# Kernel tuning notes

Measured on AMD Instinct MI355X. Metric: run time of the kernel, lower is better.

Reference implementation:

```python
import jax, jax.numpy as jnp
import numpy as np

N = 8192
H = 512
E = 262144
NUM_LAYERS = 2
LAYER_DECAY = 0.4
INIT_W = 1e-05


def setup_inputs() -> dict:
    key = jax.random.key(0)
    ks = jax.random.split(key, 6)
    x = jax.random.normal(ks[0], (N, H), dtype=jnp.float32)
    rows = jax.random.randint(ks[1], (E,), 0, N, dtype=jnp.int32)
    cols = jax.random.randint(ks[2], (E,), 0, N, dtype=jnp.int32)
    vals = jax.random.uniform(ks[3], (E,), dtype=jnp.float32)
    # near-identity init as in GSS_GNNLayer (torch Linear: y = x @ W.T + b)
    W1 = jax.random.normal(ks[4], (H, H), dtype=jnp.float32) * INIT_W + jnp.eye(H, dtype=jnp.float32)
    b1 = jnp.zeros((H,), dtype=jnp.float32)
    W2 = jax.random.normal(ks[5], (H, H), dtype=jnp.float32) * INIT_W + jnp.eye(H, dtype=jnp.float32)
    b2 = jnp.zeros((H,), dtype=jnp.float32)
    return {"x": x, "rows": rows, "cols": cols, "vals": vals,
            "W1": W1, "b1": b1, "W2": W2, "b2": b2}


def _spmm(rows, cols, vals, dense):
    # sparse [N,N] @ dense [N,H] via gather + segment-sum scatter-add
    return jax.ops.segment_sum(vals[:, None] * dense[cols], rows, num_segments=N)


def _gcn_layer(x, rows, cols, vals, W1, b1, W2, b2):
    Ax = _spmm(rows, cols, vals, x)                      # [N,H]
    pre1 = Ax @ W1.T + b1
    Ax_x = _spmm(rows, cols, vals, Ax * x)               # A(Ax * x)
    pre2 = Ax_x @ W2.T + b2
    pre = pre1 + pre2
    return pre, jax.nn.elu(pre)


def reference(x, rows, cols, vals, W1, b1, W2, b2):
    residual = None
    for _ in range(NUM_LAYERS):  # shared weights across layers, as in source
        pre, x = _gcn_layer(x, rows, cols, vals, W1, b1, W2, b2)
        if residual is not None:
            x = residual + LAYER_DECAY * x
        residual = pre
    # decoder: row-wise L2 normalize (eps=1e-12 like F.normalize), dense gram, relu
    norm = jnp.maximum(jnp.linalg.norm(x, axis=1, keepdims=True), 1e-12)
    hidden_emb = x / norm
    adj_preds = jax.nn.relu(hidden_emb @ hidden_emb.T)   # [N,N]
    return adj_preds, hidden_emb
```

## Files before the change

### kernel.cpp

```cpp
#include <hip/hip_runtime.h>

#define N_NODES 8192
#define HDIM    512
#define NEDGE   262144

typedef __attribute__((ext_vector_type(8))) short bf16x8;
typedef __attribute__((ext_vector_type(4))) float f32x4;

__device__ inline unsigned short f2bf(float f) {
  unsigned u = __float_as_uint(f);
  unsigned r = (u + 0x7FFFu + ((u >> 16) & 1u)) >> 16;
  return (unsigned short)r;
}
__device__ inline float bf2f(short s) {
  return __uint_as_float(((unsigned)(unsigned short)s) << 16);
}

__device__ inline void gload16(const void* g, void* l) {
  __builtin_amdgcn_global_load_lds(
      (const __attribute__((address_space(1))) unsigned*)g,
      (__attribute__((address_space(3))) unsigned*)l, 16, 0, 0);
}

__global__ void zero_kernel(int* __restrict__ p) {
  p[blockIdx.x * 256 + threadIdx.x] = 0;
}

__global__ void hist_kernel(const int* __restrict__ rows, int* __restrict__ counts) {
  int e = blockIdx.x * 256 + threadIdx.x;
  atomicAdd(&counts[rows[e]], 1);
}

__global__ __launch_bounds__(1024) void scan_kernel(const int* __restrict__ counts,
                                                    int* __restrict__ offs,
                                                    int* __restrict__ cursor) {
  __shared__ int s[1024];
  int tid = threadIdx.x;
  int local[8];
  int sum = 0;
#pragma unroll
  for (int i = 0; i < 8; ++i) { local[i] = counts[tid * 8 + i]; sum += local[i]; }
  s[tid] = sum;
  __syncthreads();
  for (int d = 1; d < 1024; d <<= 1) {
    int v = (tid >= d) ? s[tid - d] : 0;
    __syncthreads();
    s[tid] += v;
    __syncthreads();
  }
  int base = (tid > 0) ? s[tid - 1] : 0;
#pragma unroll
  for (int i = 0; i < 8; ++i) {
    offs[tid * 8 + i] = base;
    cursor[tid * 8 + i] = base;
    base += local[i];
  }
  if (tid == 1023) offs[8192] = base;
}

__global__ void scatter_kernel(const int* __restrict__ rows, const int* __restrict__ cols,
                               const float* __restrict__ vals, int* cursor,
                               int* __restrict__ cols_s, float* __restrict__ vals_s) {
  int e = blockIdx.x * 256 + threadIdx.x;
  int slot = atomicAdd(&cursor[rows[e]], 1);
  cols_s[slot] = cols[e];
  vals_s[slot] = vals[e];
}

template <int MODE>
__global__ __launch_bounds__(256) void spmm_bf(const int* __restrict__ offs,
                                               const int* __restrict__ cols_s,
                                               const float* __restrict__ vals_s,
                                               const short* __restrict__ Xbf,
                                               const float* __restrict__ aux,
                                               short* __restrict__ outb,
                                               short* __restrict__ prodb) {
  int row = blockIdx.x * 4 + (threadIdx.x >> 6);
  int lane = threadIdx.x & 63;
  int h0 = lane * 8;
  float acc[8] = {0.f, 0.f, 0.f, 0.f, 0.f, 0.f, 0.f, 0.f};
  int e0 = offs[row], e1 = offs[row + 1];
  for (int p = e0; p < e1; ++p) {
    float v = vals_s[p];
    int c = cols_s[p];
    bf16x8 xr = *reinterpret_cast<const bf16x8*>(Xbf + (size_t)c * HDIM + h0);
#pragma unroll
    for (int j = 0; j < 8; ++j) acc[j] = fmaf(v, bf2f(xr[j]), acc[j]);
  }
  bf16x8 o;
#pragma unroll
  for (int j = 0; j < 8; ++j) o[j] = (short)f2bf(acc[j]);
  *reinterpret_cast<bf16x8*>(outb + (size_t)row * 1024 + h0) = o;
  if (MODE != 2) {
    const float4* ap = reinterpret_cast<const float4*>(aux + (size_t)row * HDIM + h0);
    float4 a0 = ap[0], a1 = ap[1];
    float xv[8] = {a0.x, a0.y, a0.z, a0.w, a1.x, a1.y, a1.z, a1.w};
    if (MODE == 1) {
#pragma unroll
      for (int j = 0; j < 8; ++j) xv[j] = xv[j] > 0.f ? xv[j] : expm1f(xv[j]);
    }
    bf16x8 t;
#pragma unroll
    for (int j = 0; j < 8; ++j) t[j] = (short)f2bf(acc[j] * xv[j]);
    *reinterpret_cast<bf16x8*>(prodb + (size_t)row * HDIM + h0) = t;
  }
}

__global__ void cast_kernel(const float* __restrict__ src, short* __restrict__ dst,
                            int ld, int coloff) {
  int t = blockIdx.x * 256 + threadIdx.x;
  int row = t >> 6;
  int c0 = (t & 63) * 8;
  const float4* p = reinterpret_cast<const float4*>(src + (size_t)row * HDIM + c0);
  float4 a = p[0], b = p[1];
  bf16x8 o;
  o[0] = (short)f2bf(a.x); o[1] = (short)f2bf(a.y);
  o[2] = (short)f2bf(a.z); o[3] = (short)f2bf(a.w);
  o[4] = (short)f2bf(b.x); o[5] = (short)f2bf(b.y);
  o[6] = (short)f2bf(b.z); o[7] = (short)f2bf(b.w);
  *reinterpret_cast<bf16x8*>(dst + (size_t)row * ld + coloff + c0) = o;
}

__global__ void bias_kernel(const float* __restrict__ b1, const float* __restrict__ b2,
                            float* __restrict__ b12) {
  int j = blockIdx.x * 256 + threadIdx.x;
  if (j < HDIM) b12[j] = b1[j] + b2[j];
}

__global__ __launch_bounds__(256) void rownorm_kernel(const float* __restrict__ X,
                                                      float* __restrict__ outf,
                                                      short* __restrict__ outb) {
  int row = blockIdx.x * 4 + (threadIdx.x >> 6);
  int lane = threadIdx.x & 63;
  int h0 = lane * 8;
  const float4* p = reinterpret_cast<const float4*>(X + (size_t)row * HDIM + h0);
  float4 a = p[0], b = p[1];
  float s = a.x * a.x + a.y * a.y + a.z * a.z + a.w * a.w +
            b.x * b.x + b.y * b.y + b.z * b.z + b.w * b.w;
#pragma unroll
  for (int off = 1; off < 64; off <<= 1) s += __shfl_xor(s, off, 64);
  float inv = 1.f / fmaxf(sqrtf(s), 1e-12f);
  a.x *= inv; a.y *= inv; a.z *= inv; a.w *= inv;
  b.x *= inv; b.y *= inv; b.z *= inv; b.w *= inv;
  float4* q = reinterpret_cast<float4*>(outf + (size_t)row * HDIM + h0);
  q[0] = a; q[1] = b;
  bf16x8 o;
  o[0] = (short)f2bf(a.x); o[1] = (short)f2bf(a.y);
  o[2] = (short)f2bf(a.z); o[3] = (short)f2bf(a.w);
  o[4] = (short)f2bf(b.x); o[5] = (short)f2bf(b.y);
  o[6] = (short)f2bf(b.z); o[7] = (short)f2bf(b.w);
  *reinterpret_cast<bf16x8*>(outb + (size_t)row * HDIM + h0) = o;
}

template <int MODE>
__global__ __launch_bounds__(256) void gemm_lds(const short* __restrict__ A,
                                                const short* __restrict__ B,
                                                int N, int K, int nbn,
                                                const float* __restrict__ bias,
                                                const float* __restrict__ resid,
                                                float* __restrict__ out0,
                                                short* __restrict__ out1bf) {
  __shared__ __align__(16) short la[128 * 64];
  __shared__ __align__(16) short lb[128 * 64];

  int q = gridDim.x >> 3;
  int id = (blockIdx.x & 7) * q + (blockIdx.x >> 3);
  int bn = (id % nbn) * 128;
  int bm = (id / nbn) * 128;

  int lane = threadIdx.x & 63;
  int wave = threadIdx.x >> 6;

  int rsub = lane >> 3;
  int csrc = (lane & 7) ^ rsub;
  size_t ldkB = (size_t)K * 2;
  const char* gA0 = (const char*)A + (size_t)(bm + wave * 32 + rsub) * ldkB + csrc * 16;
  const char* gB0 = (const char*)B + (size_t)(bn + wave * 32 + rsub) * ldkB + csrc * 16;
  char* lA0 = (char*)la + wave * 4096;
  char* lB0 = (char*)lb + wave * 4096;

  f32x4 zero = {0.f, 0.f, 0.f, 0.f};
  f32x4 acc[4][4];
#pragma unroll
  for (int m = 0; m < 4; ++m)
#pragma unroll
    for (int n = 0; n < 4; ++n) acc[m][n] = zero;

  int rlo = lane & 15;
  int khi = lane >> 4;
  int wm = wave >> 1, wn = wave & 1;

  for (int k0 = 0; k0 < K; k0 += 64) {
    __syncthreads();
#pragma unroll
    for (int j = 0; j < 4; ++j) {
      gload16(gA0 + (size_t)j * 8 * ldkB + (size_t)k0 * 2, lA0 + j * 1024);
      gload16(gB0 + (size_t)j * 8 * ldkB + (size_t)k0 * 2, lB0 + j * 1024);
    }
    __syncthreads();
#pragma unroll
    for (int kk = 0; kk < 2; ++kk) {
      bf16x8 av[4], bv[4];
#pragma unroll
      for (int m = 0; m < 4; ++m) {
        int ra = wm * 64 + m * 16 + rlo;
        int pc = (kk * 4 + khi) ^ (ra & 7);
        av[m] = *reinterpret_cast<const bf16x8*>((const char*)la + ra * 128 + pc * 16);
      }
#pragma unroll
      for (int n = 0; n < 4; ++n) {
        int rb = wn * 64 + n * 16 + rlo;
        int pc = (kk * 4 + khi) ^ (rb & 7);
        bv[n] = *reinterpret_cast<const bf16x8*>((const char*)lb + rb * 128 + pc * 16);
      }
#pragma unroll
      for (int m = 0; m < 4; ++m)
#pragma unroll
        for (int n = 0; n < 4; ++n)
          acc[m][n] = __builtin_amdgcn_mfma_f32_16x16x32_bf16(av[m], bv[n], acc[m][n], 0, 0, 0);
    }
  }

  int obm = bm + wm * 64;
  int obn = bn + wn * 64;
  int crow = (lane >> 4) * 4;
  int ccol = lane & 15;
#pragma unroll
  for (int n = 0; n < 4; ++n) {
    int c = obn + n * 16 + ccol;
    float bc = (MODE == 2) ? 0.f : bias[c];
#pragma unroll
    for (int m = 0; m < 4; ++m) {
#pragma unroll
      for (int v = 0; v < 4; ++v) {
        int r = obm + m * 16 + crow + v;
        size_t idx = (size_t)r * N + c;
        float val = acc[m][n][v];
        if (MODE == 0) {
          float pvl = val + bc;
          out0[idx] = pvl;
          float e = pvl > 0.f ? pvl : expm1f(pvl);
          out1bf[idx] = (short)f2bf(e);
        } else if (MODE == 1) {
          float pvl = val + bc;
          out0[idx] = resid[idx] + 0.4f * (pvl > 0.f ? pvl : expm1f(pvl));
        } else {
          out0[idx] = val > 0.f ? val : 0.f;
        }
      }
    }
  }
}

extern "C" void kernel_launch(void* const* d_in, const int* in_sizes, int n_in,
                              void* d_out, int out_size, void* d_ws, size_t ws_size,
                              hipStream_t stream) {
  const float* x  = (const float*)d_in[0];
  const int* rows = (const int*)d_in[1];
  const int* cols = (const int*)d_in[2];
  const float* vals = (const float*)d_in[3];
  const float* W1 = (const float*)d_in[4];
  const float* b1 = (const float*)d_in[5];
  const float* W2 = (const float*)d_in[6];
  const float* b2 = (const float*)d_in[7];

  float* out_adj = (float*)d_out;
  float* out_hid = out_adj + (size_t)N_NODES * N_NODES;

  char* w = (char*)d_ws;
  size_t off = 0;
  auto alloc = [&](size_t bytes) -> void* {
    void* p = w + off;
    off += (bytes + 255) & ~(size_t)255;
    return p;
  };
  int* counts   = (int*)alloc(8192 * sizeof(int));
  int* offs     = (int*)alloc(8193 * sizeof(int));
  int* cursor   = (int*)alloc(8192 * sizeof(int));
  int* cols_s   = (int*)alloc((size_t)NEDGE * sizeof(int));
  float* vals_s = (float*)alloc((size_t)NEDGE * sizeof(float));
  float* b12    = (float*)alloc(HDIM * sizeof(float));
  short* Xbf    = (short*)alloc((size_t)N_NODES * HDIM * sizeof(short));
  short* Tbf    = (short*)alloc((size_t)N_NODES * HDIM * sizeof(short));
  short* Abuf   = (short*)alloc((size_t)N_NODES * 1024 * sizeof(short));
  short* Bbuf   = (short*)alloc((size_t)512 * 1024 * sizeof(short));
  float* pre1   = (float*)alloc((size_t)N_NODES * HDIM * sizeof(float));
  float* Hf     = (float*)alloc((size_t)N_NODES * HDIM * sizeof(float));
  short* Hbuf   = (short*)alloc((size_t)N_NODES * HDIM * sizeof(short));

  zero_kernel<<<32, 256, 0, stream>>>(counts);
  hist_kernel<<<NEDGE / 256, 256, 0, stream>>>(rows, counts);
  scan_kernel<<<1, 1024, 0, stream>>>(counts, offs, cursor);
  scatter_kernel<<<NEDGE / 256, 256, 0, stream>>>(rows, cols, vals, cursor, cols_s, vals_s);

  bias_kernel<<<2, 256, 0, stream>>>(b1, b2, b12);
  cast_kernel<<<(512 * 64) / 256, 256, 0, stream>>>(W1, Bbuf, 1024, 0);
  cast_kernel<<<(512 * 64) / 256, 256, 0, stream>>>(W2, Bbuf, 1024, 512);
  cast_kernel<<<2048, 256, 0, stream>>>(x, Xbf, 512, 0);

  spmm_bf<0><<<2048, 256, 0, stream>>>(offs, cols_s, vals_s, Xbf, x, Abuf, Tbf);
  spmm_bf<2><<<2048, 256, 0, stream>>>(offs, cols_s, vals_s, Tbf, nullptr, Abuf + 512, nullptr);
  gemm_lds<0><<<256, 256, 0, stream>>>(Abuf, Bbuf, 512, 1024, 4, b12, nullptr, pre1, Xbf);

  spmm_bf<1><<<2048, 256, 0, stream>>>(offs, cols_s, vals_s, Xbf, pre1, Abuf, Tbf);
  spmm_bf<2><<<2048, 256, 0, stream>>>(offs, cols_s, vals_s, Tbf, nullptr, Abuf + 512, nullptr);
  gemm_lds<1><<<256, 256, 0, stream>>>(Abuf, Bbuf, 512, 1024, 4, b12, pre1, Hf, nullptr);

  rownorm_kernel<<<2048, 256, 0, stream>>>(Hf, out_hid, Hbuf);
  gemm_lds<2><<<4096, 256, 0, stream>>>(Hbuf, Hbuf, 8192, 512, 64, nullptr, nullptr, out_adj, nullptr);
}
```

Measured before the change: 386.1 us.

## Exploit gram symmetry in decoder GEMM and split SpMM rows across two waves

The final Hbuf·Hbuf^T GEMM now computes only tiles with bm<=bn and writes each off-diagonal tile a second time, transposed through a padded LDS staging buffer. This roughly halves the MFMA work of the largest kernel, though output writes stay the same and LDS use doubles to 64KB. Separately, the SpMM kernels assign two waves per row with 4 features per lane and unroll the edge loop by 4, exposing more independent gathers in flight.

```diff
diff --git a/kernel.cpp b/kernel.cpp
--- a/kernel.cpp
+++ b/kernel.cpp
@@ -5,6 +5,7 @@
 #define NEDGE   262144
 
 typedef __attribute__((ext_vector_type(8))) short bf16x8;
+typedef __attribute__((ext_vector_type(4))) short bf16x4;
 typedef __attribute__((ext_vector_type(4))) float f32x4;
 
 __device__ inline unsigned short f2bf(float f) {
@@ -75,34 +76,52 @@
                                                const float* __restrict__ aux,
                                                short* __restrict__ outb,
                                                short* __restrict__ prodb) {
-  int row = blockIdx.x * 4 + (threadIdx.x >> 6);
+  int wave = threadIdx.x >> 6;
+  int row = blockIdx.x * 2 + (wave >> 1);
   int lane = threadIdx.x & 63;
-  int h0 = lane * 8;
-  float acc[8] = {0.f, 0.f, 0.f, 0.f, 0.f, 0.f, 0.f, 0.f};
+  int h0 = (wave & 1) * 256 + lane * 4;
+  float acc[4] = {0.f, 0.f, 0.f, 0.f};
   int e0 = offs[row], e1 = offs[row + 1];
-  for (int p = e0; p < e1; ++p) {
+  int p = e0;
+  for (; p + 4 <= e1; p += 4) {
+    float v0 = vals_s[p],     v1 = vals_s[p + 1];
+    float v2 = vals_s[p + 2], v3 = vals_s[p + 3];
+    int c0 = cols_s[p],     c1 = cols_s[p + 1];
+    int c2 = cols_s[p + 2], c3 = cols_s[p + 3];
+    bf16x4 x0 = *reinterpret_cast<const bf16x4*>(Xbf + (size_t)c0 * HDIM + h0);
+    bf16x4 x1 = *reinterpret_cast<const bf16x4*>(Xbf + (size_t)c1 * HDIM + h0);
+    bf16x4 x2 = *reinterpret_cast<const bf16x4*>(Xbf + (size_t)c2 * HDIM + h0);
+    bf16x4 x3 = *reinterpret_cast<const bf16x4*>(Xbf + (size_t)c3 * HDIM + h0);
+#pragma unroll
+    for (int j = 0; j < 4; ++j) {
+      acc[j] = fmaf(v0, bf2f(x0[j]), acc[j]);
+      acc[j] = fmaf(v1, bf2f(x1[j]), acc[j]);
+      acc[j] = fmaf(v2, bf2f(x2[j]), acc[j]);
+      acc[j] = fmaf(v3, bf2f(x3[j]), acc[j]);
+    }
+  }
+  for (; p < e1; ++p) {
     float v = vals_s[p];
     int c = cols_s[p];
-    bf16x8 xr = *reinterpret_cast<const bf16x8*>(Xbf + (size_t)c * HDIM + h0);
-#pragma unroll
-    for (int j = 0; j < 8; ++j) acc[j] = fmaf(v, bf2f(xr[j]), acc[j]);
-  }
-  bf16x8 o;
-#pragma unroll
-  for (int j = 0; j < 8; ++j) o[j] = (short)f2bf(acc[j]);
-  *reinterpret_cast<bf16x8*>(outb + (size_t)row * 1024 + h0) = o;
+    bf16x4 xr = *reinterpret_cast<const bf16x4*>(Xbf + (size_t)c * HDIM + h0);
+#pragma unroll
+    for (int j = 0; j < 4; ++j) acc[j] = fmaf(v, bf2f(xr[j]), acc[j]);
+  }
+  bf16x4 o;
+#pragma unroll
+  for (int j = 0; j < 4; ++j) o[j] = (short)f2bf(acc[j]);
+  *reinterpret_cast<bf16x4*>(outb + (size_t)row * 1024 + h0) = o;
   if (MODE != 2) {
-    const float4* ap = reinterpret_cast<const float4*>(aux + (size_t)row * HDIM + h0);
-    float4 a0 = ap[0], a1 = ap[1];
-    float xv[8] = {a0.x, a0.y, a0.z, a0.w, a1.x, a1.y, a1.z, a1.w};
+    float4 a0 = *reinterpret_cast<const float4*>(aux + (size_t)row * HDIM + h0);
+    float xv[4] = {a0.x, a0.y, a0.z, a0.w};
     if (MODE == 1) {
 #pragma unroll
-      for (int j = 0; j < 8; ++j) xv[j] = xv[j] > 0.f ? xv[j] : expm1f(xv[j]);
-    }
-    bf16x8 t;
-#pragma unroll
-    for (int j = 0; j < 8; ++j) t[j] = (short)f2bf(acc[j] * xv[j]);
-    *reinterpret_cast<bf16x8*>(prodb + (size_t)row * HDIM + h0) = t;
+      for (int j = 0; j < 4; ++j) xv[j] = xv[j] > 0.f ? xv[j] : expm1f(xv[j]);
+    }
+    bf16x4 t;
+#pragma unroll
+    for (int j = 0; j < 4; ++j) t[j] = (short)f2bf(acc[j] * xv[j]);
+    *reinterpret_cast<bf16x4*>(prodb + (size_t)row * HDIM + h0) = t;
   }
 }
 
@@ -160,13 +179,17 @@
                                                 const float* __restrict__ resid,
                                                 float* __restrict__ out0,
                                                 short* __restrict__ out1bf) {
-  __shared__ __align__(16) short la[128 * 64];
-  __shared__ __align__(16) short lb[128 * 64];
+  __shared__ __align__(16) char smem[65536];
+  short* la = (short*)smem;
+  short* lb = (short*)(smem + 32768);
+  float* tbuf = (float*)smem;
 
   int q = gridDim.x >> 3;
   int id = (blockIdx.x & 7) * q + (blockIdx.x >> 3);
-  int bn = (id % nbn) * 128;
-  int bm = (id / nbn) * 128;
+  int bnI = id % nbn, bmI = id / nbn;
+  if (MODE == 2 && bmI > bnI) return;
+  int bn = bnI * 128;
+  int bm = bmI * 128;
 
   int lane = threadIdx.x & 63;
   int wave = threadIdx.x >> 6;
@@ -248,6 +271,36 @@
           out0[idx] = val > 0.f ? val : 0.f;
         }
       }
+    }
+  }
+
+  if (MODE == 2 && bmI < bnI) {
+#pragma unroll
+    for (int h = 0; h < 2; ++h) {
+      __syncthreads();
+      if (wn == h) {
+#pragma unroll
+        for (int n = 0; n < 4; ++n) {
+#pragma unroll
+          for (int m = 0; m < 4; ++m) {
+            float4 vv;
+            vv.x = fmaxf(acc[m][n][0], 0.f);
+            vv.y = fmaxf(acc[m][n][1], 0.f);
+            vv.z = fmaxf(acc[m][n][2], 0.f);
+            vv.w = fmaxf(acc[m][n][3], 0.f);
+            *reinterpret_cast<float4*>(tbuf + (size_t)(n * 16 + ccol) * 132 +
+                                       wm * 64 + m * 16 + crow) = vv;
+          }
+        }
+      }
+      __syncthreads();
+      int i = threadIdx.x >> 2;
+      int j0 = (threadIdx.x & 3) * 32;
+      float* dst = out0 + (size_t)(bn + h * 64 + i) * N + bm + j0;
+      const float* srcb = tbuf + (size_t)i * 132 + j0;
+#pragma unroll
+      for (int jj = 0; jj < 32; jj += 4)
+        *reinterpret_cast<float4*>(dst + jj) = *reinterpret_cast<const float4*>(srcb + jj);
     }
   }
 }
@@ -298,12 +351,12 @@
   cast_kernel<<<(512 * 64) / 256, 256, 0, stream>>>(W2, Bbuf, 1024, 512);
   cast_kernel<<<2048, 256, 0, stream>>>(x, Xbf, 512, 0);
 
-  spmm_bf<0><<<2048, 256, 0, stream>>>(offs, cols_s, vals_s, Xbf, x, Abuf, Tbf);
-  spmm_bf<2><<<2048, 256, 0, stream>>>(offs, cols_s, vals_s, Tbf, nullptr, Abuf + 512, nullptr);
+  spmm_bf<0><<<4096, 256, 0, stream>>>(offs, cols_s, vals_s, Xbf, x, Abuf, Tbf);
+  spmm_bf<2><<<4096, 256, 0, stream>>>(offs, cols_s, vals_s, Tbf, nullptr, Abuf + 512, nullptr);
   gemm_lds<0><<<256, 256, 0, stream>>>(Abuf, Bbuf, 512, 1024, 4, b12, nullptr, pre1, Xbf);
 
-  spmm_bf<1><<<2048, 256, 0, stream>>>(offs, cols_s, vals_s, Xbf, pre1, Abuf, Tbf);
-  spmm_bf<2><<<2048, 256, 0, stream>>>(offs, cols_s, vals_s, Tbf, nullptr, Abuf + 512, nullptr);
+  spmm_bf<1><<<4096, 256, 0, stream>>>(offs, cols_s, vals_s, Xbf, pre1, Abuf, Tbf);
+  spmm_bf<2><<<4096, 256, 0, stream>>>(offs, cols_s, vals_s, Tbf, nullptr, Abuf + 512, nullptr);
   gemm_lds<1><<<256, 256, 0, stream>>>(Abuf, Bbuf, 512, 1024, 4, b12, pre1, Hf, nullptr);
 
   rownorm_kernel<<<2048, 256, 0, stream>>>(Hf, out_hid, Hbuf);
```

After: 484.1 us. +25.4%, slower.
